# Kernel tuning notes

Hardware: AMD Instinct MI355X
Metric: run time of the kernel (lower is better)

## Reference

```python
import jax, jax.numpy as jnp
import numpy as np

B, N, E, H, LIT, SEM, OUT = 32, 512, 128, 64, 64, 64, 64
T_FWD, T_REV = 3, 3
NEG = 1e20


def setup_inputs() -> dict:
    key = jax.random.key(0)
    ks = jax.random.split(key, 20)
    f = lambda k, sh: jax.random.normal(k, sh, dtype=jnp.float32) * 0.05
    cfg1 = jax.random.bernoulli(ks[0], 0.05, (B, N, N)).astype(jnp.float32)
    cfg2 = jax.random.bernoulli(ks[1], 0.05, (B, N, N)).astype(jnp.float32)
    return dict(
        CFG1ST=cfg1, LFG1ST=jnp.zeros((B, N, N), jnp.float32),
        LITERAL1ST=f(ks[2], (B, N, LIT)), SEMANTIC1ST=f(ks[3], (B, N, SEM)),
        CFG2ND=cfg2, LFG2ND=jnp.zeros((B, N, N), jnp.float32),
        LITERAL2ND=f(ks[4], (B, N, LIT)), SEMANTIC2ND=f(ks[5], (B, N, SEM)),
        W_lit1=f(ks[6], (LIT, H)), gru_k1=f(ks[7], (SEM, 3 * H)),
        gru_rk1=f(ks[8], (H, 3 * H)), gru_b1=jnp.zeros((2, 3 * H), jnp.float32),
        W_lit2=f(ks[9], (LIT, H)), gru_k2=f(ks[10], (SEM, 3 * H)),
        gru_rk2=f(ks[11], (H, 3 * H)), gru_b2=jnp.zeros((2, 3 * H), jnp.float32),
        a1_w=f(ks[12], (E, 1)), a1_b=jnp.zeros((1,), jnp.float32),
        a2_w=f(ks[13], (E, 1)), a2_b=jnp.zeros((1,), jnp.float32),
        W_g=f(ks[14], (E, E)),
        W_out=f(ks[15], (E, OUT)), b_out=jnp.zeros((OUT,), jnp.float32),
    )


def _gru_seq(x, k, rk, b):
    """Keras GRU (reset_after=True, tanh/sigmoid), return_sequences. x:[B,T,D] -> [B,T,H]."""
    xp = jnp.einsum('btd,dh->bth', x, k) + b[0]  # [B,T,3H]
    xz, xr, xh = jnp.split(xp, 3, axis=-1)

    h0 = jnp.zeros((x.shape[0], rk.shape[0]), x.dtype)

    def step(h, xs):
        xz_t, xr_t, xh_t = xs
        rec = h @ rk + b[1]
        rz, rr, rh = jnp.split(rec, 3, axis=-1)
        z = jax.nn.sigmoid(xz_t + rz)
        r = jax.nn.sigmoid(xr_t + rr)
        hh = jnp.tanh(xh_t + r * rh)
        h = z * h + (1.0 - z) * hh
        return h, h

    xs = (xz.transpose(1, 0, 2), xr.transpose(1, 0, 2), xh.transpose(1, 0, 2))
    _, seq = jax.lax.scan(step, h0, xs)
    return seq.transpose(1, 0, 2)


def _graph_pass(wh, A, a1_w, a1_b, a2_w, a2_b, W_g, steps):
    """GAT-like propagation. wh:[B,N,E], A:[B,N,N]."""
    mask = A * NEG - NEG  # 0 where edge, -1e20 where no edge
    for _ in range(steps):
        ah1 = wh @ a1_w + a1_b                    # [B,N,1]
        ah2 = wh @ a2_w + a2_b                    # [B,N,1]
        eij = ah1 + jnp.swapaxes(ah2, 1, 2)       # [B,N,N]
        aij = jax.nn.softmax(jax.nn.leaky_relu(eij, 0.2) + mask, axis=-1)
        attn = aij * A
        trans = jnp.einsum('bij,bjd->bid', attn, wh @ W_g)
        wh = jax.nn.elu(wh + trans)
    return wh


def reference(CFG1ST, LFG1ST, LITERAL1ST, SEMANTIC1ST,
              CFG2ND, LFG2ND, LITERAL2ND, SEMANTIC2ND,
              W_lit1, gru_k1, gru_rk1, gru_b1,
              W_lit2, gru_k2, gru_rk2, gru_b2,
              a1_w, a1_b, a2_w, a2_b, W_g, W_out, b_out):
    # TRAINING=False: dropout layers are identity.
    def data(lit, sem, Wl, k, rk, b):
        l = jax.nn.relu(lit @ Wl)                 # [B,N,H]
        s = _gru_seq(sem, k, rk, b)               # [B,N,H]
        return jnp.concatenate([l, s], axis=-1)   # [B,N,E]

    def embed(x, A):
        fwd = _graph_pass(jax.nn.relu(x), A, a1_w, a1_b, a2_w, a2_b, W_g, T_FWD)
        rev = _graph_pass(jax.nn.relu(x), jnp.swapaxes(A, 1, 2), a1_w, a1_b, a2_w, a2_b, W_g, T_REV)
        mid = jnp.sum(fwd + rev, axis=1)          # [B,E]
        return mid @ W_out + b_out                # [B,OUT]

    e1 = embed(data(LITERAL1ST, SEMANTIC1ST, W_lit1, gru_k1, gru_rk1, gru_b1), CFG1ST)
    e2 = embed(data(LITERAL2ND, SEMANTIC2ND, W_lit2, gru_k2, gru_rk2, gru_b2), CFG2ND)

    n1 = e1 / jnp.maximum(jnp.linalg.norm(e1, axis=1, keepdims=True), 1e-12)
    n2 = e2 / jnp.maximum(jnp.linalg.norm(e2, axis=1, keepdims=True), 1e-12)
    cos = jnp.sum(n1 * n2, axis=1)
    # tf cosine_similarity returns -cos; label = -(cosin - 1)/2 = (1 + cos)/2
    return (1.0 + cos) / 2.0
```

## Files before the change

### kernel.cpp

```cpp
#include <hip/hip_runtime.h>
#include <hip/hip_bf16.h>

#define BB 32
#define NNODE 512
#define EE 128
#define MAXDEG 64

typedef float v2f __attribute__((ext_vector_type(2)));
__device__ __forceinline__ v2f fma2(v2f a, v2f b, v2f c) {
  return __builtin_elementwise_fma(a, b, c);
}

__device__ __forceinline__ float sigm(float x) { return 1.0f / (1.0f + __expf(-x)); }
__device__ __forceinline__ float tanh_f(float x) {
  x = fminf(20.f, fmaxf(-20.f, x));
  float t = __expf(-2.f * x);
  return (1.f - t) / (1.f + t);
}

#define LDS_BARRIER() asm volatile("s_waitcnt lgkmcnt(0)\n\ts_barrier" ::: "memory")

__global__ __launch_bounds__(64, 1) void k_data(
    const float* __restrict__ lit1, const float* __restrict__ sem1,
    const float* __restrict__ lit2, const float* __restrict__ sem2,
    const float* __restrict__ wl1, const float* __restrict__ gk1,
    const float* __restrict__ gb1, const float* __restrict__ wl2,
    const float* __restrict__ gk2, const float* __restrict__ gb2,
    float* __restrict__ wh, float* __restrict__ xp) {
  __shared__ float stage[64 * 65];
  int bid = blockIdx.x;
  int rowblk = bid >> 1, half = bid & 1;
  int grow0 = rowblk * 64;
  int side = grow0 >> 14;
  int lrow0 = grow0 & 16383;
  const float* lit = side ? lit2 : lit1;
  const float* sem = side ? sem2 : sem1;
  const float* wl = side ? wl2 : wl1;
  const float* gk = side ? gk2 : gk1;
  const float* gb = side ? gb2 : gb1;
  int tid = threadIdx.x;

  {
    const float4* lit4 = (const float4*)(lit + (size_t)lrow0 * 64);
#pragma unroll
    for (int p = 0; p < 16; ++p) {
      int s = p * 64 + tid;
      int r = s >> 4, q = s & 15;
      float4 v = lit4[r * 16 + q];
      stage[r * 65 + 4 * q + 0] = v.x;
      stage[r * 65 + 4 * q + 1] = v.y;
      stage[r * 65 + 4 * q + 2] = v.z;
      stage[r * 65 + 4 * q + 3] = v.w;
    }
    v2f acc[16];
#pragma unroll
    for (int c = 0; c < 16; ++c) acc[c] = (v2f){0.f, 0.f};
    const float4* wl4 = (const float4*)wl;
    for (int i = 0; i < 64; ++i) {
      float rv = stage[tid * 65 + i];
      v2f rv2 = {rv, rv};
#pragma unroll
      for (int c4 = 0; c4 < 8; ++c4) {
        float4 w = wl4[i * 16 + half * 8 + c4];
        acc[2 * c4 + 0] = fma2(rv2, (v2f){w.x, w.y}, acc[2 * c4 + 0]);
        acc[2 * c4 + 1] = fma2(rv2, (v2f){w.z, w.w}, acc[2 * c4 + 1]);
      }
    }
    float4* w0 = (float4*)wh + ((size_t)(2 * side) * 16384 + lrow0 + tid) * 32;
    float4* w1 =
        (float4*)wh + ((size_t)(2 * side + 1) * 16384 + lrow0 + tid) * 32;
#pragma unroll
    for (int c4 = 0; c4 < 8; ++c4) {
      float4 o;
      o.x = fmaxf(acc[2 * c4].x, 0.f);
      o.y = fmaxf(acc[2 * c4].y, 0.f);
      o.z = fmaxf(acc[2 * c4 + 1].x, 0.f);
      o.w = fmaxf(acc[2 * c4 + 1].y, 0.f);
      w0[half * 8 + c4] = o;
      w1[half * 8 + c4] = o;
    }
  }
  {
    const float4* sem4 = (const float4*)(sem + (size_t)lrow0 * 64);
#pragma unroll
    for (int p = 0; p < 16; ++p) {
      int s = p * 64 + tid;
      int r = s >> 4, q = s & 15;
      float4 v = sem4[r * 16 + q];
      stage[r * 65 + 4 * q + 0] = v.x;
      stage[r * 65 + 4 * q + 1] = v.y;
      stage[r * 65 + 4 * q + 2] = v.z;
      stage[r * 65 + 4 * q + 3] = v.w;
    }
    v2f acc2[48];
#pragma unroll
    for (int c = 0; c < 48; ++c)
      acc2[c] = (v2f){gb[half * 96 + 2 * c], gb[half * 96 + 2 * c + 1]};
    const float4* gk4 = (const float4*)gk;
    for (int i = 0; i < 64; ++i) {
      float rv = stage[tid * 65 + i];
      v2f rv2 = {rv, rv};
#pragma unroll
      for (int c4 = 0; c4 < 24; ++c4) {
        float4 w = gk4[i * 48 + half * 24 + c4];
        acc2[2 * c4 + 0] = fma2(rv2, (v2f){w.x, w.y}, acc2[2 * c4 + 0]);
        acc2[2 * c4 + 1] = fma2(rv2, (v2f){w.z, w.w}, acc2[2 * c4 + 1]);
      }
    }
    float4* xp4 = (float4*)xp;
    int grow = grow0 + tid;
#pragma unroll
    for (int c4 = 0; c4 < 24; ++c4) {
      float4 o;
      o.x = acc2[2 * c4].x;
      o.y = acc2[2 * c4].y;
      o.z = acc2[2 * c4 + 1].x;
      o.w = acc2[2 * c4 + 1].y;
      xp4[(size_t)grow * 48 + half * 24 + c4] = o;
    }
  }
}

__global__ __launch_bounds__(256, 1) void k_gru_cf(
    const float* __restrict__ xp, const float* __restrict__ rk1,
    const float* __restrict__ b1, const float* __restrict__ rk2,
    const float* __restrict__ b2, float* __restrict__ wh,
    const float* __restrict__ A1, const float* __restrict__ A2,
    int* __restrict__ counts, int* __restrict__ edges) {
  int tid = threadIdx.x;
  if (blockIdx.x < 64) {
    int blk = blockIdx.x;
    int side = blk >> 5, b = blk & 31;
    int wave = tid >> 6;
    int lane = tid & 63;
    int jj = (lane & 15) + 16 * wave;
    int ks = (lane >> 4) & 3;
    const float* rk = side ? rk2 : rk1;
    const float* bbp = side ? b2 : b1;
    v2f wz[8], wr[8], wv[8];
#pragma unroll
    for (int i = 0; i < 8; ++i) {
      int r0 = 16 * ks + 2 * i, r1 = r0 + 1;
      wz[i] = (v2f){rk[r0 * 192 + jj], rk[r1 * 192 + jj]};
      wr[i] = (v2f){rk[r0 * 192 + 64 + jj], rk[r1 * 192 + 64 + jj]};
      wv[i] = (v2f){rk[r0 * 192 + 128 + jj], rk[r1 * 192 + 128 + jj]};
    }
    float bz = bbp[192 + jj], brr = bbp[192 + 64 + jj], bv = bbp[192 + 128 + jj];

    __shared__ float hs[2][64];
    __shared__ float xpb[2][16 * 192];
    if (tid < 64) hs[0][tid] = 0.f;

    const float* xpr = xp + (size_t)(side * 16384 + b * 512) * 192;
    float* w0 = wh + ((size_t)(2 * side) * 16384 + b * 512) * 128 + 64 + jj;
    float* w1 = wh + ((size_t)(2 * side + 1) * 16384 + b * 512) * 128 + 64 + jj;

    {
      const float4* src = (const float4*)xpr;
      float4* dst = (float4*)xpb[0];
#pragma unroll
      for (int q = 0; q < 3; ++q) dst[q * 256 + tid] = src[q * 256 + tid];
    }
    __syncthreads();

    float hout[16];
    int cur = 0;
    for (int tc = 0; tc < 32; ++tc) {
      float4 pf0, pf1, pf2;
      if (tc + 1 < 32) {
        const float4* src = (const float4*)(xpr + (size_t)(tc + 1) * 3072);
        pf0 = src[0 * 256 + tid];
        pf1 = src[1 * 256 + tid];
        pf2 = src[2 * 256 + tid];
      }
#pragma unroll
      for (int tt = 0; tt < 16; ++tt) {
        int t = tc * 16 + tt;
        int hb = t & 1;
        const float* hsrc = hs[hb];
        const float* xc = &xpb[cur][tt * 192];
        float cxz = xc[jj], cxr = xc[64 + jj], cxv = xc[128 + jj];
        float hold = hsrc[jj];
        const float4* h4 = (const float4*)(hsrc + 16 * ks);
        v2f az = {0.f, 0.f}, ar = {0.f, 0.f}, av = {0.f, 0.f};
#pragma unroll
        for (int c = 0; c < 4; ++c) {
          float4 h = h4[c];
          v2f hlo = {h.x, h.y}, hhi = {h.z, h.w};
          az = fma2(hlo, wz[2 * c], az);
          az = fma2(hhi, wz[2 * c + 1], az);
          ar = fma2(hlo, wr[2 * c], ar);
          ar = fma2(hhi, wr[2 * c + 1], ar);
          av = fma2(hlo, wv[2 * c], av);
          av = fma2(hhi, wv[2 * c + 1], av);
        }
        float saz = az.x + az.y, sar = ar.x + ar.y, sav = av.x + av.y;
        saz += __shfl_xor(saz, 16, 64);
        saz += __shfl_xor(saz, 32, 64);
        sar += __shfl_xor(sar, 16, 64);
        sar += __shfl_xor(sar, 32, 64);
        sav += __shfl_xor(sav, 16, 64);
        sav += __shfl_xor(sav, 32, 64);
        float z = sigm(cxz + saz + bz);
        float r = sigm(cxr + sar + brr);
        float hh = tanh_f(cxv + r * (sav + bv));
        float hnew = fmaf(z, hold - hh, hh);
        hout[tt] = hnew;
        if (ks == 0) hs[hb ^ 1][jj] = hnew;
        LDS_BARRIER();
      }
      if (ks == 0) {
        size_t ro = (size_t)(tc * 16) * 128;
#pragma unroll
        for (int tt = 0; tt < 16; ++tt) {
          float rv = fmaxf(hout[tt], 0.f);
          w0[ro + (size_t)tt * 128] = rv;
          w1[ro + (size_t)tt * 128] = rv;
        }
      }
      if (tc + 1 < 32) {
        float4* dst = (float4*)xpb[cur ^ 1];
        dst[0 * 256 + tid] = pf0;
        dst[1 * 256 + tid] = pf1;
        dst[2 * 256 + tid] = pf2;
        LDS_BARRIER();
      }
      cur ^= 1;
    }
    return;
  }
  int bid = blockIdx.x - 64;
  int t = tid;
  if (bid < 512) {
    int s = bid >> 8, b = (bid >> 3) & 31, ch = bid & 7;
    const float* A = s ? A2 : A1;
    const float4* A4 = (const float4*)(A + ((size_t)b * 512 + ch * 64) * 512);
    __shared__ int crow[64];
    if (t < 64) crow[t] = 0;
    __syncthreads();
    int* efwd =
        edges + (size_t)(2 * s) * 1048576 + ((size_t)b * 512 + ch * 64) * 64;
#pragma unroll
    for (int it = 0; it < 32; ++it) {
      int idx = it * 256 + t;
      int r = idx >> 7, c4 = idx & 127;
      float4 v = A4[idx];
      float vv[4] = {v.x, v.y, v.z, v.w};
#pragma unroll
      for (int e = 0; e < 4; ++e) {
        if (vv[e] != 0.f) {
          int pos = atomicAdd(&crow[r], 1);
          if (pos < MAXDEG) efwd[r * 64 + pos] = 4 * c4 + e;
        }
      }
    }
    __syncthreads();
    if (t < 64)
      counts[(2 * s) * 16384 + b * 512 + ch * 64 + t] = min(crow[t], MAXDEG);
  } else {
    int bid2 = bid - 512;
    int s = bid2 >> 8, b = (bid2 >> 3) & 31, cch = bid2 & 7;
    const float* A = s ? A2 : A1;
    __shared__ int ccol[64];
    if (t < 64) ccol[t] = 0;
    __syncthreads();
    int lane = t & 63, rg = t >> 6;
    int c = cch * 64 + lane;
    int* erev = edges + (size_t)(2 * s + 1) * 1048576 + ((size_t)b * 512) * 64;
    const float* Ab = A + (size_t)b * 512 * 512;
    for (int it = 0; it < 128; ++it) {
      int r = it * 4 + rg;
      float a = Ab[(size_t)r * 512 + c];
      if (a != 0.f) {
        int pos = atomicAdd(&ccol[lane], 1);
        if (pos < MAXDEG) erev[(size_t)c * 64 + pos] = r;
      }
    }
    __syncthreads();
    if (t < 64)
      counts[(2 * s + 1) * 16384 + b * 512 + cch * 64 + t] =
          min(ccol[t], MAXDEG);
  }
}

__global__ __launch_bounds__(64, 1) void k_whg(
    const float* __restrict__ wh, const float* __restrict__ Wg,
    const float* __restrict__ a1w, const float* __restrict__ a1b,
    const float* __restrict__ a2w, const float* __restrict__ a2b,
    unsigned int* __restrict__ whg, float* __restrict__ ah1,
    float* __restrict__ ah2) {
  __shared__ float stage[64 * 129];
  int B = blockIdx.x;
  int xcd = B & 7, slot = B >> 3;
  int grp = xcd + 8 * (slot >> 3);
  int sub = slot & 7;
  int rowbase = grp * 512 + sub * 64;
  int tid = threadIdx.x;
  const float4* wh4 = (const float4*)(wh + (size_t)rowbase * 128);
#pragma unroll
  for (int p = 0; p < 32; ++p) {
    int s = p * 64 + tid;
    int r = s >> 5, q = s & 31;
    float4 v = wh4[r * 32 + q];
    stage[r * 129 + 4 * q + 0] = v.x;
    stage[r * 129 + 4 * q + 1] = v.y;
    stage[r * 129 + 4 * q + 2] = v.z;
    stage[r * 129 + 4 * q + 3] = v.w;
  }
  v2f acc[64];
#pragma unroll
  for (int c = 0; c < 64; ++c) acc[c] = (v2f){0.f, 0.f};
  float p1 = a1b[0], p2 = a2b[0];
  const float4* Wg4 = (const float4*)Wg;
  for (int i = 0; i < 128; ++i) {
    float rv = stage[tid * 129 + i];
    v2f rv2 = {rv, rv};
    p1 = fmaf(rv, a1w[i], p1);
    p2 = fmaf(rv, a2w[i], p2);
#pragma unroll
    for (int c4 = 0; c4 < 32; ++c4) {
      float4 w = Wg4[i * 32 + c4];
      acc[2 * c4 + 0] = fma2(rv2, (v2f){w.x, w.y}, acc[2 * c4 + 0]);
      acc[2 * c4 + 1] = fma2(rv2, (v2f){w.z, w.w}, acc[2 * c4 + 1]);
    }
  }
  int grow = rowbase + tid;
  uint2* o2 = (uint2*)(whg + (size_t)grow * 64);
#pragma unroll
  for (int c4 = 0; c4 < 32; c4 += 2) {
    __hip_bfloat162 A =
        __float22bfloat162_rn(make_float2(acc[c4].x, acc[c4].y));
    __hip_bfloat162 Bv =
        __float22bfloat162_rn(make_float2(acc[c4 + 1].x, acc[c4 + 1].y));
    uint2 pk;
    pk.x = *(unsigned int*)&A;
    pk.y = *(unsigned int*)&Bv;
    o2[c4 >> 1] = pk;
  }
  ah1[grow] = p1;
  ah2[grow] = p2;
}

__global__ __launch_bounds__(256, 1) void k_attn(
    float* __restrict__ wh, const unsigned int* __restrict__ whg,
    const float* __restrict__ ah1, const float* __restrict__ ah2,
    const int* __restrict__ counts, const int* __restrict__ edges) {
  int B = blockIdx.x;
  int xcd = B & 7, slot = B >> 3;
  int grp = xcd + 8 * (slot >> 7);
  int sub = slot & 127;
  int row = grp * 512 + sub * 4 + (threadIdx.x >> 6);
  int lane = threadIdx.x & 63;
  int st = row >> 14;
  int loc = row & 16383;
  int base = row & ~511;
  int cnt = counts[row];
  const int* ed = edges + (size_t)st * 1048576 + (size_t)loc * 64;
  int jk = lane < cnt ? ed[lane] : 0;
  float a1v = ah1[row];
  float e = a1v + ah2[base + jk];
  e = e >= 0.f ? e : 0.2f * e;
  float w = lane < cnt ? __expf(e) : 0.f;
  float lsum = w;
#pragma unroll
  for (int off = 32; off; off >>= 1) lsum += __shfl_xor(lsum, off, 64);
  float inv = cnt > 0 ? 1.0f / lsum : 0.f;
  const unsigned int* wgb = whg + (size_t)base * 64;
  v2f a0 = {0.f, 0.f}, a1 = {0.f, 0.f}, a2 = {0.f, 0.f}, a3 = {0.f, 0.f};
  int k = 0;
  for (; k + 4 <= cnt; k += 4) {
    float w0 = __shfl(w, k, 64), w1 = __shfl(w, k + 1, 64);
    float w2 = __shfl(w, k + 2, 64), w3 = __shfl(w, k + 3, 64);
    int j0 = __shfl(jk, k, 64), j1 = __shfl(jk, k + 1, 64);
    int j2 = __shfl(jk, k + 2, 64), j3 = __shfl(jk, k + 3, 64);
    unsigned int d0 = wgb[(size_t)j0 * 64 + lane];
    unsigned int d1 = wgb[(size_t)j1 * 64 + lane];
    unsigned int d2 = wgb[(size_t)j2 * 64 + lane];
    unsigned int d3 = wgb[(size_t)j3 * 64 + lane];
    v2f v0 = {__uint_as_float(d0 << 16), __uint_as_float(d0 & 0xffff0000u)};
    v2f v1 = {__uint_as_float(d1 << 16), __uint_as_float(d1 & 0xffff0000u)};
    v2f v2 = {__uint_as_float(d2 << 16), __uint_as_float(d2 & 0xffff0000u)};
    v2f v3 = {__uint_as_float(d3 << 16), __uint_as_float(d3 & 0xffff0000u)};
    a0 = fma2((v2f){w0, w0}, v0, a0);
    a1 = fma2((v2f){w1, w1}, v1, a1);
    a2 = fma2((v2f){w2, w2}, v2, a2);
    a3 = fma2((v2f){w3, w3}, v3, a3);
  }
  for (; k < cnt; ++k) {
    float w0 = __shfl(w, k, 64);
    int j0 = __shfl(jk, k, 64);
    unsigned int d0 = wgb[(size_t)j0 * 64 + lane];
    v2f v0 = {__uint_as_float(d0 << 16), __uint_as_float(d0 & 0xffff0000u)};
    a0 = fma2((v2f){w0, w0}, v0, a0);
  }
  v2f acc = (a0 + a1) + (a2 + a3);
  float2* wr2 = (float2*)(wh + (size_t)row * 128);
  float2 old = wr2[lane];
  float o0 = old.x + acc.x * inv;
  float o1 = old.y + acc.y * inv;
  o0 = o0 > 0.f ? o0 : __expf(o0) - 1.f;
  o1 = o1 > 0.f ? o1 : __expf(o1) - 1.f;
  wr2[lane] = make_float2(o0, o1);
}

__global__ __launch_bounds__(256, 1) void k_tail(const float* __restrict__ wh,
                                                 const float* __restrict__ Wout,
                                                 const float* __restrict__ bout,
                                                 float* __restrict__ e12) {
  int sb = blockIdx.x;
  int side = sb >> 5, b = sb & 31;
  int t = threadIdx.x;
  int c = t & 127, half = t >> 7;
  __shared__ float part[2][128];
  __shared__ float mid[128];
  size_t s0 = ((size_t)(2 * side) * 16384 + b * 512) * 128;
  size_t s1 = ((size_t)(2 * side + 1) * 16384 + b * 512) * 128;
  float sum = 0.f;
  int r0 = half * 256;
  for (int r = r0; r < r0 + 256; ++r) {
    sum += wh[s0 + (size_t)r * 128 + c] + wh[s1 + (size_t)r * 128 + c];
  }
  part[half][c] = sum;
  __syncthreads();
  if (t < 128) mid[t] = part[0][t] + part[1][t];
  __syncthreads();
  if (t < 64) {
    float acc = bout[t];
    for (int k2 = 0; k2 < 128; ++k2) acc = fmaf(mid[k2], Wout[k2 * 64 + t], acc);
    e12[sb * 64 + t] = acc;
  }
}

__global__ void k_cos(const float* __restrict__ e12, float* __restrict__ out) {
  int b = threadIdx.x;
  if (b >= 32) return;
  const float* e1 = e12 + b * 64;
  const float* e2 = e12 + 2048 + b * 64;
  float d = 0.f, n1 = 0.f, n2 = 0.f;
  for (int o = 0; o < 64; ++o) {
    float a = e1[o], c = e2[o];
    d = fmaf(a, c, d);
    n1 = fmaf(a, a, n1);
    n2 = fmaf(c, c, n2);
  }
  float nn = fmaxf(sqrtf(n1), 1e-12f) * fmaxf(sqrtf(n2), 1e-12f);
  out[b] = 0.5f * (1.f + d / nn);
}

extern "C" void kernel_launch(void* const* d_in, const int* in_sizes, int n_in,
                              void* d_out, int out_size, void* d_ws,
                              size_t ws_size, hipStream_t stream) {
  const float* CFG1 = (const float*)d_in[0];
  const float* LIT1 = (const float*)d_in[2];
  const float* SEM1 = (const float*)d_in[3];
  const float* CFG2 = (const float*)d_in[4];
  const float* LIT2 = (const float*)d_in[6];
  const float* SEM2 = (const float*)d_in[7];
  const float* WL1 = (const float*)d_in[8];
  const float* GK1 = (const float*)d_in[9];
  const float* GRK1 = (const float*)d_in[10];
  const float* GB1 = (const float*)d_in[11];
  const float* WL2 = (const float*)d_in[12];
  const float* GK2 = (const float*)d_in[13];
  const float* GRK2 = (const float*)d_in[14];
  const float* GB2 = (const float*)d_in[15];
  const float* A1W = (const float*)d_in[16];
  const float* A1B = (const float*)d_in[17];
  const float* A2W = (const float*)d_in[18];
  const float* A2B = (const float*)d_in[19];
  const float* WG = (const float*)d_in[20];
  const float* WOUT = (const float*)d_in[21];
  const float* BOUT = (const float*)d_in[22];

  float* ws = (float*)d_ws;
  float* wh = ws;
  float* xp = wh + 8388608;
  unsigned int* whg = (unsigned int*)(xp + 6291456);
  float* ah1 = (float*)(whg + 4194304);
  float* ah2 = ah1 + 65536;
  float* e12 = ah2 + 65536;
  int* counts = (int*)(e12 + 4096);
  int* edges = counts + 65536;

  k_data<<<1024, 64, 0, stream>>>(LIT1, SEM1, LIT2, SEM2, WL1, GK1, GB1, WL2,
                                  GK2, GB2, wh, xp);
  k_gru_cf<<<1088, 256, 0, stream>>>(xp, GRK1, GB1, GRK2, GB2, wh, CFG1, CFG2,
                                     counts, edges);
  for (int step = 0; step < 3; ++step) {
    k_whg<<<1024, 64, 0, stream>>>(wh, WG, A1W, A1B, A2W, A2B, whg, ah1, ah2);
    k_attn<<<16384, 256, 0, stream>>>(wh, whg, ah1, ah2, counts, edges);
  }
  k_tail<<<64, 256, 0, stream>>>(wh, WOUT, BOUT, e12);
  k_cos<<<1, 64, 0, stream>>>(e12, (float*)d_out);
}
```

Baseline: 770.8 us.

## Run GRU recurrence in a single wavefront with full per-lane dot products

The GRU recurrence block now uses one wave of 64 lanes instead of four waves that split the K dimension. Each lane holds the full 64-row column of recurrent weights in registers and computes the whole dot product. This removes the cross-lane shuffle reductions and the per-timestep workgroup barriers. Sigmoid and tanh also switch to hardware reciprocal approximations. The trade-off is four times more serial FMA work per lane, much higher register use, and slightly lower accuracy in the activations.

```diff
diff --git a/kernel.cpp b/kernel.cpp
--- a/kernel.cpp
+++ b/kernel.cpp
@@ -11,14 +11,14 @@
   return __builtin_elementwise_fma(a, b, c);
 }
 
-__device__ __forceinline__ float sigm(float x) { return 1.0f / (1.0f + __expf(-x)); }
-__device__ __forceinline__ float tanh_f(float x) {
+__device__ __forceinline__ float sigm_fast(float x) {
+  return __builtin_amdgcn_rcpf(1.0f + __expf(-x));
+}
+__device__ __forceinline__ float tanh_fast(float x) {
   x = fminf(20.f, fmaxf(-20.f, x));
   float t = __expf(-2.f * x);
-  return (1.f - t) / (1.f + t);
-}
-
-#define LDS_BARRIER() asm volatile("s_waitcnt lgkmcnt(0)\n\ts_barrier" ::: "memory")
+  return (1.f - t) * __builtin_amdgcn_rcpf(1.f + t);
+}
 
 __global__ __launch_bounds__(64, 1) void k_data(
     const float* __restrict__ lit1, const float* __restrict__ sem1,
@@ -129,27 +129,28 @@
     int* __restrict__ counts, int* __restrict__ edges) {
   int tid = threadIdx.x;
   if (blockIdx.x < 64) {
+    if (tid >= 64) return;
     int blk = blockIdx.x;
     int side = blk >> 5, b = blk & 31;
-    int wave = tid >> 6;
-    int lane = tid & 63;
-    int jj = (lane & 15) + 16 * wave;
-    int ks = (lane >> 4) & 3;
+    int jj = tid;
     const float* rk = side ? rk2 : rk1;
     const float* bbp = side ? b2 : b1;
-    v2f wz[8], wr[8], wv[8];
-#pragma unroll
-    for (int i = 0; i < 8; ++i) {
-      int r0 = 16 * ks + 2 * i, r1 = r0 + 1;
-      wz[i] = (v2f){rk[r0 * 192 + jj], rk[r1 * 192 + jj]};
-      wr[i] = (v2f){rk[r0 * 192 + 64 + jj], rk[r1 * 192 + 64 + jj]};
-      wv[i] = (v2f){rk[r0 * 192 + 128 + jj], rk[r1 * 192 + 128 + jj]};
-    }
-    float bz = bbp[192 + jj], brr = bbp[192 + 64 + jj], bv = bbp[192 + 128 + jj];
-
-    __shared__ float hs[2][64];
+    v2f wz[32], wr[32], wv[32];
+#pragma unroll
+    for (int p = 0; p < 32; ++p) {
+      const float* r0 = rk + (size_t)(2 * p) * 192 + jj;
+      const float* r1 = rk + (size_t)(2 * p + 1) * 192 + jj;
+      wz[p] = (v2f){r0[0], r1[0]};
+      wr[p] = (v2f){r0[64], r1[64]};
+      wv[p] = (v2f){r0[128], r1[128]};
+    }
+    float bz = bbp[192 + jj], brr = bbp[192 + 64 + jj],
+          bv = bbp[192 + 128 + jj];
+
+    __shared__ float hs[64];
     __shared__ float xpb[2][16 * 192];
-    if (tid < 64) hs[0][tid] = 0.f;
+    hs[jj] = 0.f;
+    float hold = 0.f;
 
     const float* xpr = xp + (size_t)(side * 16384 + b * 512) * 192;
     float* w0 = wh + ((size_t)(2 * side) * 16384 + b * 512) * 128 + 64 + jj;
@@ -159,32 +160,27 @@
       const float4* src = (const float4*)xpr;
       float4* dst = (float4*)xpb[0];
 #pragma unroll
-      for (int q = 0; q < 3; ++q) dst[q * 256 + tid] = src[q * 256 + tid];
-    }
-    __syncthreads();
-
+      for (int q = 0; q < 12; ++q) dst[q * 64 + jj] = src[q * 64 + jj];
+    }
+    asm volatile("s_waitcnt lgkmcnt(0)" ::: "memory");
+
+    int cur = 0;
     float hout[16];
-    int cur = 0;
     for (int tc = 0; tc < 32; ++tc) {
-      float4 pf0, pf1, pf2;
+      float4 pf[12];
       if (tc + 1 < 32) {
         const float4* src = (const float4*)(xpr + (size_t)(tc + 1) * 3072);
-        pf0 = src[0 * 256 + tid];
-        pf1 = src[1 * 256 + tid];
-        pf2 = src[2 * 256 + tid];
+#pragma unroll
+        for (int q = 0; q < 12; ++q) pf[q] = src[q * 64 + jj];
       }
 #pragma unroll
       for (int tt = 0; tt < 16; ++tt) {
-        int t = tc * 16 + tt;
-        int hb = t & 1;
-        const float* hsrc = hs[hb];
         const float* xc = &xpb[cur][tt * 192];
         float cxz = xc[jj], cxr = xc[64 + jj], cxv = xc[128 + jj];
-        float hold = hsrc[jj];
-        const float4* h4 = (const float4*)(hsrc + 16 * ks);
+        const float4* h4 = (const float4*)hs;
         v2f az = {0.f, 0.f}, ar = {0.f, 0.f}, av = {0.f, 0.f};
 #pragma unroll
-        for (int c = 0; c < 4; ++c) {
+        for (int c = 0; c < 16; ++c) {
           float4 h = h4[c];
           v2f hlo = {h.x, h.y}, hhi = {h.z, h.w};
           az = fma2(hlo, wz[2 * c], az);
@@ -195,35 +191,25 @@
           av = fma2(hhi, wv[2 * c + 1], av);
         }
         float saz = az.x + az.y, sar = ar.x + ar.y, sav = av.x + av.y;
-        saz += __shfl_xor(saz, 16, 64);
-        saz += __shfl_xor(saz, 32, 64);
-        sar += __shfl_xor(sar, 16, 64);
-        sar += __shfl_xor(sar, 32, 64);
-        sav += __shfl_xor(sav, 16, 64);
-        sav += __shfl_xor(sav, 32, 64);
-        float z = sigm(cxz + saz + bz);
-        float r = sigm(cxr + sar + brr);
-        float hh = tanh_f(cxv + r * (sav + bv));
+        float z = sigm_fast(cxz + saz + bz);
+        float r = sigm_fast(cxr + sar + brr);
+        float hh = tanh_fast(cxv + r * (sav + bv));
         float hnew = fmaf(z, hold - hh, hh);
         hout[tt] = hnew;
-        if (ks == 0) hs[hb ^ 1][jj] = hnew;
-        LDS_BARRIER();
-      }
-      if (ks == 0) {
-        size_t ro = (size_t)(tc * 16) * 128;
-#pragma unroll
-        for (int tt = 0; tt < 16; ++tt) {
-          float rv = fmaxf(hout[tt], 0.f);
-          w0[ro + (size_t)tt * 128] = rv;
-          w1[ro + (size_t)tt * 128] = rv;
-        }
+        hold = hnew;
+        hs[jj] = hnew;
+      }
+      size_t ro = (size_t)(tc * 16) * 128;
+#pragma unroll
+      for (int tt = 0; tt < 16; ++tt) {
+        float rv = fmaxf(hout[tt], 0.f);
+        w0[ro + (size_t)tt * 128] = rv;
+        w1[ro + (size_t)tt * 128] = rv;
       }
       if (tc + 1 < 32) {
         float4* dst = (float4*)xpb[cur ^ 1];
-        dst[0 * 256 + tid] = pf0;
-        dst[1 * 256 + tid] = pf1;
-        dst[2 * 256 + tid] = pf2;
-        LDS_BARRIER();
+#pragma unroll
+        for (int q = 0; q < 12; ++q) dst[q * 64 + jj] = pf[q];
       }
       cur ^= 1;
     }
```

Result: slower. 805.5 us (+4.5%).
